# Kernel tuning notes

Measured on AMD Instinct MI355X. Metric: run time of the kernel, lower is better.

## Reference

```python
import jax, jax.numpy as jnp
import numpy as np

T_TAYLOR = 10  # T=10 in OrthogonalGCNConvLayer
N_ORTH_LAYERS = 10


def _taylor_expm(S):
    # exp(S) truncated at T terms; S is skew-symmetric -> approx orthogonal
    I = jnp.eye(S.shape[0], dtype=S.dtype)
    term = I
    acc = I
    for k in range(1, T_TAYLOR + 1):
        term = term @ S / k
        acc = acc + term
    return acc


def setup_inputs() -> dict:
    key = jax.random.key(0)
    ks = jax.random.split(key, 8)
    N = 200_000
    E = 1_200_000
    x = jax.random.normal(ks[0], (N, 1), dtype=jnp.float32)
    edge_index = jax.random.randint(ks[1], (2, E), 0, N, dtype=jnp.int64)
    edge_weight = jax.random.uniform(ks[2], (E,), dtype=jnp.float32)
    W0 = jax.random.normal(ks[3], (1, 64), dtype=jnp.float32) * 0.1
    b0 = jnp.zeros((64,), dtype=jnp.float32)
    # small scale so the truncated matrix exponential stays well-conditioned
    W_orth = jax.random.normal(ks[4], (N_ORTH_LAYERS, 64, 64), dtype=jnp.float32) * 0.05
    W11 = jax.random.normal(ks[5], (64, 1), dtype=jnp.float32) * 0.1
    b11 = jnp.zeros((1,), dtype=jnp.float32)
    return {"x": x, "edge_index": edge_index, "edge_weight": edge_weight,
            "W0": W0, "b0": b0, "W_orth": W_orth, "W11": W11, "b11": b11}


def reference(x, edge_index, edge_weight, W0, b0, W_orth, W11, b11):
    N = x.shape[0]
    row, col = edge_index[0], edge_index[1]
    # add_self_loops=True: append (i,i) edges with weight 1 (PyG gcn_norm fill_value=1)
    loop = jnp.arange(N, dtype=row.dtype)
    row_f = jnp.concatenate([row, loop])
    col_f = jnp.concatenate([col, loop])
    w_f = jnp.concatenate([edge_weight, jnp.ones((N,), dtype=edge_weight.dtype)])
    # degree via scatter-sum over target nodes (matches scatter(..., col, reduce='sum'))
    deg = jax.ops.segment_sum(w_f, col_f, num_segments=N)
    deg_inv_sqrt = jnp.where(deg > 0, jax.lax.rsqrt(jnp.maximum(deg, 1e-30)), 0.0)
    norm = deg_inv_sqrt[row_f] * w_f * deg_inv_sqrt[col_f]  # [E+N]

    def propagate(h):
        # gather messages from source nodes, scale, scatter-add at targets
        return jax.ops.segment_sum(norm[:, None] * h[row_f], col_f, num_segments=N)

    # block 0: GCNConv(1 -> 64)
    h = propagate(x @ W0) + b0
    # blocks 1..10: Orthogonal GCN conv (64 -> 64), Identity activation,
    # no residual / bias; orthogonal weight = truncated expm of skew(W)
    for k in range(N_ORTH_LAYERS):
        Wk = W_orth[k]
        orth = _taylor_expm(Wk - Wk.T)
        h = propagate(h) @ orth
    # block 11: GCNConv(64 -> 1)
    out = propagate(h @ W11) + b11
    return out[:, :, None]  # [N, 1, 1]
```

## Files before the change

kernel.cpp:

```cpp
#include <hip/hip_runtime.h>
#include <hip/hip_bf16.h>


#define TPB 256
#define CSH 11
#define CSZ 2048
#define CAPSH 14
#define FSH 7
#define FBPB 16
#define PE 4096

__device__ void v_part(float* __restrict__ smem,
                       const float* __restrict__ W_orth,
                       const float* __restrict__ W11,
                       const float* __restrict__ W0,
                       const float* __restrict__ b0,
                       float* __restrict__ st,
                       int khi, int klo, bool first) {
    const int l = threadIdx.x;
    if (l >= 64) return;
    float* S  = smem;
    float* tl = smem + 4160;
    float u = first ? W11[l] : st[2 + l];
    for (int k = khi; k >= klo; --k) {
        const float* Wk = W_orth + (size_t)k * 4096;
        #pragma unroll 1
        for (int i = 0; i < 64; ++i)
            S[i * 65 + l] = Wk[i * 64 + l] - Wk[l * 64 + i];
        float term = u, acc = u;
        for (int t = 1; t <= 10; ++t) {
            tl[l] = term;
            float p = 0.f;
            #pragma unroll 16
            for (int j = 0; j < 64; ++j)
                p = fmaf(S[l * 65 + j], tl[j], p);
            term = p / (float)t;
            acc += term;
        }
        u = acc;
    }
    if (klo == 0) {
        float a = W0[l] * u, b = b0[l] * u;
        #pragma unroll
        for (int off = 32; off; off >>= 1) {
            a += __shfl_down(a, off);
            b += __shfl_down(b, off);
        }
        if (l == 0) { st[0] = a; st[1] = b; }
    } else {
        st[2 + l] = u;
    }
}

__global__ __launch_bounds__(TPB) void k_part(
        const int* __restrict__ ei, const float* __restrict__ w,
        int E, int nchunk, int CB,
        int* __restrict__ pos, int2* __restrict__ recA,
        const float* __restrict__ W_orth,
        const float* __restrict__ W11, float* __restrict__ scal) {
    __shared__ float smem[8192];
    __shared__ int hist[128], rank[128], gbase[128];
    __shared__ int sscan[128], starts[129];
    const int me = blockIdx.x, t = threadIdx.x;
    if (me == nchunk) { v_part(smem, W_orth, W11, nullptr, nullptr, scal, 9, 4, true); return; }
    int2* staged = (int2*)smem;
    if (t < 128) { hist[t] = 0; rank[t] = 0; }
    __syncthreads();
    const int e0 = me * PE, e1 = min(E, e0 + PE);
    const int nE = e1 - e0;
    for (int e = e0 + t; e < e1; e += TPB)
        atomicAdd(&hist[ei[E + e] >> CSH], 1);
    __syncthreads();
    if (t < 128) sscan[t] = hist[t];
    __syncthreads();
    for (int o = 1; o < 128; o <<= 1) {
        int v = (t < 128 && t >= o) ? sscan[t - o] : 0;
        __syncthreads();
        if (t < 128) sscan[t] += v;
        __syncthreads();
    }
    if (t < 128) starts[t] = sscan[t] - hist[t];
    if (t == 127) starts[128] = sscan[127];
    if (t < CB && hist[t] > 0)
        gbase[t] = (t << CAPSH) + atomicAdd(&pos[t], hist[t]);
    __syncthreads();
    for (int e = e0 + t; e < e1; e += TPB) {
        int src = ei[e], c = ei[E + e];
        float wv = w[e];
        int b = c >> CSH;
        int r = atomicAdd(&rank[b], 1);
        staged[starts[b] + r] = make_int2(src | ((c & (CSZ - 1)) << 18),
                                          __float_as_int(wv));
    }
    __syncthreads();
    for (int s = t; s < nE; s += TPB) {
        int lo = 0, hi = 128;
        while (hi - lo > 1) {
            int mid = (lo + hi) >> 1;
            if (starts[mid] <= s) lo = mid; else hi = mid;
        }
        recA[gbase[lo] + (s - starts[lo])] = staged[s];
    }
}

__global__ __launch_bounds__(TPB) void k_sub(
        const int* __restrict__ pos, const int2* __restrict__ recA,
        int2* __restrict__ recB,
        int* __restrict__ binStart, int* __restrict__ binEnd,
        const float* __restrict__ x, float* __restrict__ dis,
        float* __restrict__ d2, float* __restrict__ u0,
        int N, int CB,
        const float* __restrict__ W_orth,
        const float* __restrict__ W0, const float* __restrict__ b0,
        float* __restrict__ scal) {
    __shared__ float smem[6144];
    __shared__ int h16[16], st16[17], run16[16], bh16[16], bst16[17];
    const int b = blockIdx.x, t = threadIdx.x;
    if (b == CB) { v_part(smem, W_orth, nullptr, W0, b0, scal, 3, 0, false); return; }
    int2* staged = (int2*)smem;
    float* acc   = smem + 4096;
    const int cnt = pos[b];
    const int2* rin = recA + ((size_t)b << CAPSH);
    int2* rout      = recB + ((size_t)b << CAPSH);
    for (int i = t; i < CSZ; i += TPB) acc[i] = 0.f;
    if (t < 16) h16[t] = 0;
    __syncthreads();
    for (int k = t; k < cnt; k += TPB) {
        int2 rc = rin[k];
        int cl = rc.x >> 18;
        atomicAdd(&h16[cl >> FSH], 1);
        atomicAdd(&acc[cl], __int_as_float(rc.y));
    }
    __syncthreads();
    if (t == 0) { int s = 0; for (int j = 0; j < 16; ++j) { st16[j] = s; s += h16[j]; } st16[16] = s; }
    __syncthreads();
    if (t < 16) {
        binStart[b * FBPB + t] = (b << CAPSH) + st16[t];
        binEnd  [b * FBPB + t] = (b << CAPSH) + st16[t + 1];
        run16[t] = st16[t];
    }
    for (int i = t; i < CSZ; i += TPB) {
        int node = (b << CSH) + i;
        if (node < N) {
            float deg = 1.0f + acc[i];
            float ds = rsqrtf(deg);
            dis[node] = ds;
            d2[node]  = 1.0f / deg;
            u0[node]  = ds * x[node];
        }
    }
    __syncthreads();
    for (int base = 0; base < cnt; base += 2048) {
        const int n = min(2048, cnt - base);
        if (t < 16) bh16[t] = 0;
        __syncthreads();
        for (int k = base + t; k < base + n; k += TPB)
            atomicAdd(&bh16[(rin[k].x >> 18) >> FSH], 1);
        __syncthreads();
        if (t == 0) { int s = 0; for (int j = 0; j < 16; ++j) { bst16[j] = s; s += bh16[j]; } bst16[16] = s; }
        __syncthreads();
        if (t < 16) bh16[t] = 0;
        __syncthreads();
        for (int k = base + t; k < base + n; k += TPB) {
            int2 rc = rin[k];
            int cl = rc.x >> 18;
            int j = cl >> FSH;
            int r = atomicAdd(&bh16[j], 1);
            staged[bst16[j] + r] =
                make_int2((rc.x & 0x3FFFF) | ((cl & 127) << 18), rc.y);
        }
        __syncthreads();
        for (int s = t; s < n; s += TPB) {
            int lo = 0, hi = 16;
            while (hi - lo > 1) {
                int mid = (lo + hi) >> 1;
                if (bst16[mid] <= s) lo = mid; else hi = mid;
            }
            rout[run16[lo] + (s - bst16[lo])] = staged[s];
        }
        __syncthreads();
        if (t < 16) run16[t] += bh16[t];
        __syncthreads();
    }
}

__global__ void k_gather(const int* __restrict__ binStart,
                         const int* __restrict__ binEnd,
                         const int2* __restrict__ rec,
                         const float* __restrict__ d2,
                         const float* __restrict__ pv, float* __restrict__ cv,
                         int N, int mode,
                         const float* __restrict__ scal,
                         const float* __restrict__ dis,
                         const float* __restrict__ b11, float* __restrict__ out) {
    const int fb = blockIdx.x, t = threadIdx.x;
    __shared__ float acc[128];
    if (t < 128) acc[t] = 0.f;
    __syncthreads();
    const int k0 = binStart[fb], k1 = binEnd[fb];
    for (int k = k0 + t; k < k1; k += TPB) {
        int2 rc = rec[k];
        atomicAdd(&acc[rc.x >> 18],
                  __int_as_float(rc.y) * pv[rc.x & 0x3FFFF]);
    }
    __syncthreads();
    if (t < 128) {
        int i = (fb << FSH) + t;
        if (i < N) {
            float up = d2[i] * (pv[i] + acc[t]);
            if (mode == 1)
                cv[i] = scal[0] * up + scal[1] * dis[i];
            else if (mode == 2)
                out[i] = up / dis[i] + b11[0];
            else
                cv[i] = up;
        }
    }
}

extern "C" void kernel_launch(void* const* d_in, const int* in_sizes, int n_in,
                              void* d_out, int out_size, void* d_ws, size_t ws_size,
                              hipStream_t stream) {
    const float* x      = (const float*)d_in[0];
    const int*   ei     = (const int*)d_in[1];
    const float* w      = (const float*)d_in[2];
    const float* W0     = (const float*)d_in[3];
    const float* b0     = (const float*)d_in[4];
    const float* W_orth = (const float*)d_in[5];
    const float* W11    = (const float*)d_in[6];
    const float* b11    = (const float*)d_in[7];

    const int N = in_sizes[0];
    const int E = in_sizes[2];
    const int CB = (N + CSZ - 1) >> CSH;
    const int nchunk = (E + PE - 1) / PE;
    const size_t cap = (size_t)CB << CAPSH;

    char* ws = (char*)d_ws;
    int2*  recA     = (int2*)ws;   ws += cap * 8;
    int2*  recB     = (int2*)ws;   ws += cap * 8;
    float* uA       = (float*)ws;  ws += (size_t)N * 4;
    float* uB       = (float*)ws;  ws += (size_t)N * 4;
    float* dis      = (float*)ws;  ws += (size_t)N * 4;
    float* d2       = (float*)ws;  ws += (size_t)N * 4;
    int*   binStart = (int*)ws;    ws += (size_t)CB * FBPB * 4;
    int*   binEnd   = (int*)ws;    ws += (size_t)CB * FBPB * 4;
    int*   pos      = (int*)ws;    ws += 128 * 4;
    float* scal     = (float*)ws;  ws += 80 * 4;

    hipMemsetAsync(pos, 0, 128 * 4, stream);
    k_part<<<nchunk + 1, TPB, 0, stream>>>(ei, w, E, nchunk, CB, pos, recA,
                                           W_orth, W11, scal);
    k_sub<<<CB + 1, TPB, 0, stream>>>(pos, recA, recB, binStart, binEnd,
                                      x, dis, d2, uA, N, CB,
                                      W_orth, W0, b0, scal);

    float* prev = uA;
    float* cur  = uB;
    for (int it = 0; it < 12; ++it) {
        int mode = (it == 0) ? 1 : (it == 11 ? 2 : 0);
        k_gather<<<CB * FBPB, TPB, 0, stream>>>(binStart, binEnd, recB, d2,
                                                prev, cur, N, mode, scal, dis,
                                                b11, (float*)d_out);
        float* tmp = prev; prev = cur; cur = tmp;
    }
}
```

Measured before the change: 323.0 us.

## Widen partition kernels to 1024 threads, vectorize loads, store bucket ids

The two partitioning kernels now launch 1024 threads per block and read edge columns, sources and weights as 128-bit vectors. Each staged record gets a byte-sized bucket id in shared memory, so the scatter-out pass looks up its bucket directly instead of binary-searching the start offsets. k_sub spreads its sub-bin histogram over per-wave copies to reduce atomic contention, and it drops the separate re-histogram pass by keeping a dedicated rank counter. The risks are lower occupancy from the larger blocks and the vector loads' assumption that each chunk's start is 16-byte aligned.

```diff
diff --git a/kernel.cpp b/kernel.cpp
--- a/kernel.cpp
+++ b/kernel.cpp
@@ -52,23 +52,35 @@
     }
 }
 
-__global__ __launch_bounds__(TPB) void k_part(
+__global__ __launch_bounds__(1024) void k_part(
         const int* __restrict__ ei, const float* __restrict__ w,
         int E, int nchunk, int CB,
         int* __restrict__ pos, int2* __restrict__ recA,
         const float* __restrict__ W_orth,
         const float* __restrict__ W11, float* __restrict__ scal) {
-    __shared__ float smem[8192];
+    __shared__ float smem[9216];
     __shared__ int hist[128], rank[128], gbase[128];
     __shared__ int sscan[128], starts[129];
     const int me = blockIdx.x, t = threadIdx.x;
     if (me == nchunk) { v_part(smem, W_orth, W11, nullptr, nullptr, scal, 9, 4, true); return; }
     int2* staged = (int2*)smem;
+    unsigned char* sb = (unsigned char*)(smem + 8192);
     if (t < 128) { hist[t] = 0; rank[t] = 0; }
     __syncthreads();
     const int e0 = me * PE, e1 = min(E, e0 + PE);
     const int nE = e1 - e0;
-    for (int e = e0 + t; e < e1; e += TPB)
+    const int nv = nE >> 2;
+    const int4*   cv4 = (const int4*)(ei + (size_t)E + e0);
+    const int4*   sv4 = (const int4*)(ei + e0);
+    const float4* wv4 = (const float4*)(w + e0);
+    for (int g = t; g < nv; g += 1024) {
+        int4 c4 = cv4[g];
+        atomicAdd(&hist[c4.x >> CSH], 1);
+        atomicAdd(&hist[c4.y >> CSH], 1);
+        atomicAdd(&hist[c4.z >> CSH], 1);
+        atomicAdd(&hist[c4.w >> CSH], 1);
+    }
+    for (int e = e0 + (nv << 2) + t; e < e1; e += 1024)
         atomicAdd(&hist[ei[E + e] >> CSH], 1);
     __syncthreads();
     if (t < 128) sscan[t] = hist[t];
@@ -84,26 +96,34 @@
     if (t < CB && hist[t] > 0)
         gbase[t] = (t << CAPSH) + atomicAdd(&pos[t], hist[t]);
     __syncthreads();
-    for (int e = e0 + t; e < e1; e += TPB) {
+    for (int g = t; g < nv; g += 1024) {
+        int4 s4 = sv4[g]; int4 c4 = cv4[g]; float4 w4 = wv4[g];
+        int b, r, p;
+        b = c4.x >> CSH; r = atomicAdd(&rank[b], 1); p = starts[b] + r;
+        staged[p] = make_int2(s4.x | ((c4.x & (CSZ - 1)) << 18), __float_as_int(w4.x)); sb[p] = (unsigned char)b;
+        b = c4.y >> CSH; r = atomicAdd(&rank[b], 1); p = starts[b] + r;
+        staged[p] = make_int2(s4.y | ((c4.y & (CSZ - 1)) << 18), __float_as_int(w4.y)); sb[p] = (unsigned char)b;
+        b = c4.z >> CSH; r = atomicAdd(&rank[b], 1); p = starts[b] + r;
+        staged[p] = make_int2(s4.z | ((c4.z & (CSZ - 1)) << 18), __float_as_int(w4.z)); sb[p] = (unsigned char)b;
+        b = c4.w >> CSH; r = atomicAdd(&rank[b], 1); p = starts[b] + r;
+        staged[p] = make_int2(s4.w | ((c4.w & (CSZ - 1)) << 18), __float_as_int(w4.w)); sb[p] = (unsigned char)b;
+    }
+    for (int e = e0 + (nv << 2) + t; e < e1; e += 1024) {
         int src = ei[e], c = ei[E + e];
-        float wv = w[e];
         int b = c >> CSH;
         int r = atomicAdd(&rank[b], 1);
-        staged[starts[b] + r] = make_int2(src | ((c & (CSZ - 1)) << 18),
-                                          __float_as_int(wv));
-    }
-    __syncthreads();
-    for (int s = t; s < nE; s += TPB) {
-        int lo = 0, hi = 128;
-        while (hi - lo > 1) {
-            int mid = (lo + hi) >> 1;
-            if (starts[mid] <= s) lo = mid; else hi = mid;
-        }
-        recA[gbase[lo] + (s - starts[lo])] = staged[s];
-    }
-}
-
-__global__ __launch_bounds__(TPB) void k_sub(
+        int p = starts[b] + r;
+        staged[p] = make_int2(src | ((c & (CSZ - 1)) << 18), __float_as_int(w[e]));
+        sb[p] = (unsigned char)b;
+    }
+    __syncthreads();
+    for (int s = t; s < nE; s += 1024) {
+        int b = sb[s];
+        recA[gbase[b] + (s - starts[b])] = staged[s];
+    }
+}
+
+__global__ __launch_bounds__(1024) void k_sub(
         const int* __restrict__ pos, const int2* __restrict__ recA,
         int2* __restrict__ recB,
         int* __restrict__ binStart, int* __restrict__ binEnd,
@@ -113,24 +133,29 @@
         const float* __restrict__ W_orth,
         const float* __restrict__ W0, const float* __restrict__ b0,
         float* __restrict__ scal) {
-    __shared__ float smem[6144];
-    __shared__ int h16[16], st16[17], run16[16], bh16[16], bst16[17];
+    __shared__ float smem[6656];
+    __shared__ int hw[16][17];
+    __shared__ int h16[16], st16[17], run16[16], rk16[16], bst16[17], bcnt[16];
     const int b = blockIdx.x, t = threadIdx.x;
     if (b == CB) { v_part(smem, W_orth, nullptr, W0, b0, scal, 3, 0, false); return; }
     int2* staged = (int2*)smem;
     float* acc   = smem + 4096;
+    unsigned char* sb = (unsigned char*)(smem + 6144);
+    const int wid = t >> 6;
     const int cnt = pos[b];
     const int2* rin = recA + ((size_t)b << CAPSH);
     int2* rout      = recB + ((size_t)b << CAPSH);
-    for (int i = t; i < CSZ; i += TPB) acc[i] = 0.f;
-    if (t < 16) h16[t] = 0;
-    __syncthreads();
-    for (int k = t; k < cnt; k += TPB) {
+    for (int i = t; i < CSZ; i += 1024) acc[i] = 0.f;
+    if (t < 272) ((int*)hw)[t] = 0;
+    __syncthreads();
+    for (int k = t; k < cnt; k += 1024) {
         int2 rc = rin[k];
         int cl = rc.x >> 18;
-        atomicAdd(&h16[cl >> FSH], 1);
+        atomicAdd(&hw[wid][cl >> FSH], 1);
         atomicAdd(&acc[cl], __int_as_float(rc.y));
     }
+    __syncthreads();
+    if (t < 16) { int s = 0; for (int q = 0; q < 16; ++q) s += hw[q][t]; h16[t] = s; }
     __syncthreads();
     if (t == 0) { int s = 0; for (int j = 0; j < 16; ++j) { st16[j] = s; s += h16[j]; } st16[16] = s; }
     __syncthreads();
@@ -139,7 +164,7 @@
         binEnd  [b * FBPB + t] = (b << CAPSH) + st16[t + 1];
         run16[t] = st16[t];
     }
-    for (int i = t; i < CSZ; i += TPB) {
+    for (int i = t; i < CSZ; i += 1024) {
         int node = (b << CSH) + i;
         if (node < N) {
             float deg = 1.0f + acc[i];
@@ -152,34 +177,31 @@
     __syncthreads();
     for (int base = 0; base < cnt; base += 2048) {
         const int n = min(2048, cnt - base);
-        if (t < 16) bh16[t] = 0;
-        __syncthreads();
-        for (int k = base + t; k < base + n; k += TPB)
-            atomicAdd(&bh16[(rin[k].x >> 18) >> FSH], 1);
-        __syncthreads();
-        if (t == 0) { int s = 0; for (int j = 0; j < 16; ++j) { bst16[j] = s; s += bh16[j]; } bst16[16] = s; }
-        __syncthreads();
-        if (t < 16) bh16[t] = 0;
-        __syncthreads();
-        for (int k = base + t; k < base + n; k += TPB) {
+        if (t < 272) ((int*)hw)[t] = 0;
+        __syncthreads();
+        for (int k = base + t; k < base + n; k += 1024)
+            atomicAdd(&hw[wid][(rin[k].x >> 18) >> FSH], 1);
+        __syncthreads();
+        if (t < 16) { int s = 0; for (int q = 0; q < 16; ++q) s += hw[q][t]; bcnt[t] = s; rk16[t] = 0; }
+        __syncthreads();
+        if (t == 0) { int s = 0; for (int j = 0; j < 16; ++j) { bst16[j] = s; s += bcnt[j]; } bst16[16] = s; }
+        __syncthreads();
+        for (int k = base + t; k < base + n; k += 1024) {
             int2 rc = rin[k];
             int cl = rc.x >> 18;
             int j = cl >> FSH;
-            int r = atomicAdd(&bh16[j], 1);
-            staged[bst16[j] + r] =
-                make_int2((rc.x & 0x3FFFF) | ((cl & 127) << 18), rc.y);
-        }
-        __syncthreads();
-        for (int s = t; s < n; s += TPB) {
-            int lo = 0, hi = 16;
-            while (hi - lo > 1) {
-                int mid = (lo + hi) >> 1;
-                if (bst16[mid] <= s) lo = mid; else hi = mid;
-            }
-            rout[run16[lo] + (s - bst16[lo])] = staged[s];
-        }
-        __syncthreads();
-        if (t < 16) run16[t] += bh16[t];
+            int r = atomicAdd(&rk16[j], 1);
+            int p = bst16[j] + r;
+            staged[p] = make_int2((rc.x & 0x3FFFF) | ((cl & 127) << 18), rc.y);
+            sb[p] = (unsigned char)j;
+        }
+        __syncthreads();
+        for (int s = t; s < n; s += 1024) {
+            int j = sb[s];
+            rout[run16[j] + (s - bst16[j])] = staged[s];
+        }
+        __syncthreads();
+        if (t < 16) run16[t] += bcnt[t];
         __syncthreads();
     }
 }
@@ -249,11 +271,11 @@
     float* scal     = (float*)ws;  ws += 80 * 4;
 
     hipMemsetAsync(pos, 0, 128 * 4, stream);
-    k_part<<<nchunk + 1, TPB, 0, stream>>>(ei, w, E, nchunk, CB, pos, recA,
-                                           W_orth, W11, scal);
-    k_sub<<<CB + 1, TPB, 0, stream>>>(pos, recA, recB, binStart, binEnd,
-                                      x, dis, d2, uA, N, CB,
-                                      W_orth, W0, b0, scal);
+    k_part<<<nchunk + 1, 1024, 0, stream>>>(ei, w, E, nchunk, CB, pos, recA,
+                                            W_orth, W11, scal);
+    k_sub<<<CB + 1, 1024, 0, stream>>>(pos, recA, recB, binStart, binEnd,
+                                       x, dis, d2, uA, N, CB,
+                                       W_orth, W0, b0, scal);
 
     float* prev = uA;
     float* cur  = uB;
```

Result: faster. 309.3 us (-4.2%).
